# Performance work log

Hardware: AMD Instinct MI355X
Metric: run time of the kernel (lower is better)

The kernel has to match this reference:

```python
import jax, jax.numpy as jnp
import numpy as np

B, LQ, LK, D = 16, 2048, 2048, 64
TEMPERATURE = 8.0  # sqrt(d_k)


def setup_inputs() -> dict:
    key = jax.random.key(0)
    kq, kk, kv, km = jax.random.split(key, 4)
    q = jax.random.normal(kq, (B, LQ, D), dtype=jnp.float32)
    k = jax.random.normal(kk, (B, LK, D), dtype=jnp.float32)
    v = jax.random.normal(kv, (B, LK, D), dtype=jnp.float32)
    mask = jax.random.randint(km, (B, LQ, LK), 0, 2).astype(jnp.bool_)
    return {"q": q, "k": k, "v": v, "mask": mask}


def reference(q, k, v, mask):
    # attn = bmm(q, k^T) / temperature  -> [B, LQ, LK]
    attn = jnp.einsum("bqd,bkd->bqk", q, k) / TEMPERATURE
    attn = jnp.where(mask, -jnp.inf, attn)
    attn = jax.nn.softmax(attn, axis=2)
    out = jnp.einsum("bqk,bkd->bqd", attn, v)  # [B, LQ, D]
    return out, attn
```

## Files before the change

kernel.cpp:

```cpp
#include <hip/hip_runtime.h>
#include <hip/hip_bf16.h>

namespace {
constexpr int kB = 16;
constexpr int kLQ = 2048;
constexpr int kLK = 2048;
constexpr int kD = 64;
constexpr float kLog2e = 1.44269504088896340736f;
constexpr int kQT = 64;
constexpr int kKT = 512;
constexpr int kKStrB = 144;
constexpr int kMStrB = 40;
constexpr int kBStrB = 144;
constexpr int kChunk = 256;
constexpr int kEStrB = 528;
}

using short8 = __attribute__((ext_vector_type(8))) short;
using f32x4 = __attribute__((ext_vector_type(4))) float;

union S8U { short8 v; unsigned u[4]; };

static __device__ __forceinline__ unsigned pk2(float lo, float hi) {
    __hip_bfloat162 h = __float22bfloat162_rn(float2{lo, hi});
    unsigned short a = __builtin_bit_cast(unsigned short, h.x);
    unsigned short b = __builtin_bit_cast(unsigned short, h.y);
    return (unsigned)a | ((unsigned)b << 16);
}

__global__ __launch_bounds__(256, 4) void k1_qke(
    const float* __restrict__ qg, const float* __restrict__ kg,
    const void* __restrict__ maskg, float* __restrict__ attng,
    float* __restrict__ outg)
{
    __shared__ __align__(16) unsigned char s_kst[32 * kKStrB];
    __shared__ __align__(16) unsigned char s_mst[64 * kMStrB];
    __shared__ __align__(16) unsigned char s_bnc[4][16 * kBStrB];
    __shared__ int s_flag;

    const int tid = threadIdx.x;
    const int wave = tid >> 6;
    const int lane = tid & 63;
    const int r16 = lane & 15;
    const int g = lane >> 4;

    const int blk = blockIdx.x;
    const int b = blk >> 7;
    const int kt = (blk >> 5) & 3;
    const int qt = blk & 31;
    const int rows0 = qt * kQT;
    const int c0 = kt * kKT;

    if (tid < 64) {
        unsigned w = ((const unsigned*)maskg)[tid];
        unsigned long long bal = __ballot((w & 0xFFFFFF00u) != 0u);
        if (tid == 0) s_flag = (bal != 0ull) ? 1 : 0;
    }
    __syncthreads();
    const bool mask_byte = (s_flag != 0);
    const unsigned char* mask_u8 = (const unsigned char*)maskg;
    const int* mask_i32 = (const int*)maskg;

    short8 q0, q1;
    {
        const float4* qp = (const float4*)(qg + ((size_t)b * kLQ + rows0 + wave * 16 + r16) * kD);
        const float s = 0.125f * kLog2e;
        float4 x0 = qp[2*g + 0], x1 = qp[2*g + 1];
        float4 x2 = qp[2*g + 8], x3 = qp[2*g + 9];
        x0 *= s; x1 *= s; x2 *= s; x3 *= s;
        S8U a, c;
        a.u[0] = pk2(x0.x, x0.y); a.u[1] = pk2(x0.z, x0.w);
        a.u[2] = pk2(x1.x, x1.y); a.u[3] = pk2(x1.z, x1.w);
        c.u[0] = pk2(x2.x, x2.y); c.u[1] = pk2(x2.z, x2.w);
        c.u[2] = pk2(x3.x, x3.y); c.u[3] = pk2(x3.z, x3.w);
        q0 = a.v; q1 = c.v;
    }

    float wsum = 0.f;

    for (int sub = 0; sub < kKT / 32; ++sub) {
        const int csub = c0 + sub * 32;
        {
            const int krow = tid >> 3;
            const int d8 = (tid & 7) * 8;
            const float4* kp = (const float4*)(kg + ((size_t)b * kLK + csub + krow) * kD + d8);
            float4 y0 = kp[0], y1 = kp[1];
            S8U p;
            p.u[0] = pk2(y0.x, y0.y); p.u[1] = pk2(y0.z, y0.w);
            p.u[2] = pk2(y1.x, y1.y); p.u[3] = pk2(y1.z, y1.w);
            *(short8*)(s_kst + krow * kKStrB + d8 * 2) = p.v;
        }
        {
            const int mrow = tid >> 2;
            const int mc = (tid & 3) * 8;
            unsigned long long f;
            if (mask_byte) {
                f = *(const unsigned long long*)(mask_u8 +
                        ((size_t)b * kLQ + rows0 + mrow) * (size_t)kLK + csub + mc);
            } else {
                const int* mp = mask_i32 + ((size_t)b * kLQ + rows0 + mrow) * (size_t)kLK + csub + mc;
                const int4 m0 = *(const int4*)mp;
                const int4 m1 = *(const int4*)(mp + 4);
                f  = (m0.x ? 1ull : 0ull)       | (m0.y ? 1ull << 8 : 0ull)
                   | (m0.z ? 1ull << 16 : 0ull) | (m0.w ? 1ull << 24 : 0ull)
                   | (m1.x ? 1ull << 32 : 0ull) | (m1.y ? 1ull << 40 : 0ull)
                   | (m1.z ? 1ull << 48 : 0ull) | (m1.w ? 1ull << 56 : 0ull);
            }
            *(unsigned long long*)(s_mst + mrow * kMStrB + mc) = f;
        }
        __syncthreads();

        const short8 kA0 = *(const short8*)(s_kst + r16 * kKStrB + g * 16);
        const short8 kA1 = *(const short8*)(s_kst + r16 * kKStrB + 64 + g * 16);
        const short8 kB0 = *(const short8*)(s_kst + (16 + r16) * kKStrB + g * 16);
        const short8 kB1 = *(const short8*)(s_kst + (16 + r16) * kKStrB + 64 + g * 16);
        f32x4 accA = {0.f, 0.f, 0.f, 0.f}, accB = {0.f, 0.f, 0.f, 0.f};
        accA = __builtin_amdgcn_mfma_f32_16x16x32_bf16(kA0, q0, accA, 0, 0, 0);
        accA = __builtin_amdgcn_mfma_f32_16x16x32_bf16(kA1, q1, accA, 0, 0, 0);
        accB = __builtin_amdgcn_mfma_f32_16x16x32_bf16(kB0, q0, accB, 0, 0, 0);
        accB = __builtin_amdgcn_mfma_f32_16x16x32_bf16(kB1, q1, accB, 0, 0, 0);

        const unsigned mwA = *(const unsigned*)(s_mst + (wave * 16 + r16) * kMStrB + 4 * g);
        const unsigned mwB = *(const unsigned*)(s_mst + (wave * 16 + r16) * kMStrB + 16 + 4 * g);
        f32x4 eA, eB;
#pragma unroll
        for (int r = 0; r < 4; ++r) {
            eA[r] = ((mwA >> (8*r)) & 0xFFu) ? 0.f : __builtin_amdgcn_exp2f(accA[r]);
            eB[r] = ((mwB >> (8*r)) & 0xFFu) ? 0.f : __builtin_amdgcn_exp2f(accB[r]);
        }
        wsum += (eA[0] + eA[1]) + (eA[2] + eA[3]) + (eB[0] + eB[1]) + (eB[2] + eB[3]);
        *(f32x4*)(s_bnc[wave] + r16 * kBStrB + g * 16) = eA;
        *(f32x4*)(s_bnc[wave] + r16 * kBStrB + 64 + g * 16) = eB;
        __syncthreads();

        {
            const int row = tid >> 2;
            const int cseg = tid & 3;
            const unsigned char* src = s_bnc[row >> 4] + (row & 15) * kBStrB + cseg * 32;
            const f32x4 v0 = *(const f32x4*)src;
            const f32x4 v1 = *(const f32x4*)(src + 16);
            float* dst = attng + ((size_t)b * kLQ + rows0 + row) * (size_t)kLK + csub + cseg * 8;
            *(f32x4*)dst = v0;
            *(f32x4*)(dst + 4) = v1;
        }
    }
    wsum += __shfl_xor(wsum, 16, 64);
    wsum += __shfl_xor(wsum, 32, 64);
    if (g == 0)
        outg[((size_t)b * kLQ + rows0 + wave * 16 + r16) * kD + kt] = wsum;
}

__global__ __launch_bounds__(512, 2) void k2_norm_pv(
    const float* __restrict__ vg, float* __restrict__ attng,
    float* __restrict__ outg)
{
    __shared__ __align__(16) unsigned char s_e[16 * kEStrB];
    __shared__ float s_red[16][kD];
    __shared__ float s_rinv[16];

    const int tid = threadIdx.x;
    const int wave = tid >> 6;
    const int lane = tid & 63;
    const int r16 = lane & 15;
    const int g = lane >> 4;

    const int blk = blockIdx.x;
    const int b = blk >> 7;
    const int row0 = (blk & 127) * 16;

    if (tid < 64) {
        const int r = tid >> 2, p = tid & 3;
        float ps = outg[((size_t)b * kLQ + row0 + r) * kD + p];
        ps += __shfl_xor(ps, 1, 64);
        ps += __shfl_xor(ps, 2, 64);
        if (p == 0) s_rinv[r] = __builtin_amdgcn_rcpf(ps);
    }
    __syncthreads();

    const int d0 = (wave & 3) * 16;
    const int kh = wave >> 2;
    f32x4 acc = {0.f, 0.f, 0.f, 0.f};
    const float* vbase = vg + (size_t)b * kLK * kD + d0 + r16;

    for (int chunk = 0; chunk < kLK / kChunk; ++chunk) {
        const int c0 = chunk * kChunk;
        {
            const int row = tid >> 5;
            const int cc = tid & 31;
            const float rinv = s_rinv[row];
            float* ap = attng + ((size_t)b * kLQ + row0 + row) * (size_t)kLK + c0 + cc * 8;
            f32x4 e0 = *(const f32x4*)ap;
            f32x4 e1 = *(const f32x4*)(ap + 4);
            e0 *= rinv; e1 *= rinv;
            *(f32x4*)ap = e0;
            *(f32x4*)(ap + 4) = e1;
            S8U p;
            p.u[0] = pk2(e0[0], e0[1]); p.u[1] = pk2(e0[2], e0[3]);
            p.u[2] = pk2(e1[0], e1[1]); p.u[3] = pk2(e1[2], e1[3]);
            *(short8*)(s_e + row * kEStrB + cc * 16) = p.v;
        }
        __syncthreads();
#pragma unroll
        for (int s = 0; s < 4; ++s) {
            const int kk = kh * 128 + s * 32 + 8 * g;
            const short8 af = *(const short8*)(s_e + r16 * kEStrB + kk * 2);
            const float* vp = vbase + (size_t)(c0 + kk) * kD;
            float v0 = vp[0*kD], v1 = vp[1*kD], v2 = vp[2*kD], v3 = vp[3*kD];
            float v4 = vp[4*kD], v5 = vp[5*kD], v6 = vp[6*kD], v7 = vp[7*kD];
            S8U bv;
            bv.u[0] = pk2(v0, v1); bv.u[1] = pk2(v2, v3);
            bv.u[2] = pk2(v4, v5); bv.u[3] = pk2(v6, v7);
            acc = __builtin_amdgcn_mfma_f32_16x16x32_bf16(af, bv.v, acc, 0, 0, 0);
        }
        __syncthreads();
    }

    if (kh == 1) {
#pragma unroll
        for (int r = 0; r < 4; ++r) s_red[4*g + r][d0 + r16] = acc[r];
    }
    __syncthreads();
    if (kh == 0) {
#pragma unroll
        for (int r = 0; r < 4; ++r) {
            const int m = 4*g + r;
            outg[((size_t)b * kLQ + row0 + m) * kD + d0 + r16] = acc[r] + s_red[m][d0 + r16];
        }
    }
}

extern "C" void kernel_launch(void* const* d_in, const int* in_sizes, int n_in,
                              void* d_out, int out_size, void* d_ws, size_t ws_size,
                              hipStream_t stream) {
    (void)in_sizes; (void)n_in; (void)out_size; (void)d_ws; (void)ws_size;
    const float* q = (const float*)d_in[0];
    const float* k = (const float*)d_in[1];
    const float* v = (const float*)d_in[2];
    const void* mask = d_in[3];
    float* out = (float*)d_out;
    float* attn = out + (size_t)kB * kLQ * kD;
    k1_qke<<<dim3(kB * 128), 256, 0, stream>>>(q, k, mask, attn, out);
    k2_norm_pv<<<dim3(kB * 128), 512, 0, stream>>>(v, attn, out);
}
```

Before: 285.4 us.

## Stage unnormalized exp scores as bf16 in workspace instead of fp32 attn

The first kernel now packs the masked exp scores to bf16 and writes them to a workspace buffer, instead of writing fp32 into the attn output. The second kernel reads these half-size values, writes the normalized fp32 attn once, and feeds the raw bf16 values to the P·V MFMA. The output is rescaled by the row reciprocal at the end. This drops the fp32 read-modify-write round trip on the large attn matrix, cutting global traffic. In exchange the attn output now carries bf16 rounding, and the raised launch-bounds occupancy targets may force register spills.

```diff
diff --git a/kernel.cpp b/kernel.cpp
--- a/kernel.cpp
+++ b/kernel.cpp
@@ -11,7 +11,7 @@
 constexpr int kKT = 512;
 constexpr int kKStrB = 144;
 constexpr int kMStrB = 40;
-constexpr int kBStrB = 144;
+constexpr int kBStrB = 72;
 constexpr int kChunk = 256;
 constexpr int kEStrB = 528;
 }
@@ -27,10 +27,14 @@
     unsigned short b = __builtin_bit_cast(unsigned short, h.y);
     return (unsigned)a | ((unsigned)b << 16);
 }
-
-__global__ __launch_bounds__(256, 4) void k1_qke(
+static __device__ __forceinline__ float bf2f(unsigned short s) {
+    unsigned u = ((unsigned)s) << 16;
+    return __builtin_bit_cast(float, u);
+}
+
+__global__ __launch_bounds__(256, 8) void k1_qke(
     const float* __restrict__ qg, const float* __restrict__ kg,
-    const void* __restrict__ maskg, float* __restrict__ attng,
+    const void* __restrict__ maskg, unsigned short* __restrict__ ews,
     float* __restrict__ outg)
 {
     __shared__ __align__(16) unsigned char s_kst[32 * kKStrB];
@@ -122,26 +126,25 @@
 
         const unsigned mwA = *(const unsigned*)(s_mst + (wave * 16 + r16) * kMStrB + 4 * g);
         const unsigned mwB = *(const unsigned*)(s_mst + (wave * 16 + r16) * kMStrB + 16 + 4 * g);
-        f32x4 eA, eB;
+        float eA[4], eB[4];
 #pragma unroll
         for (int r = 0; r < 4; ++r) {
             eA[r] = ((mwA >> (8*r)) & 0xFFu) ? 0.f : __builtin_amdgcn_exp2f(accA[r]);
             eB[r] = ((mwB >> (8*r)) & 0xFFu) ? 0.f : __builtin_amdgcn_exp2f(accB[r]);
         }
         wsum += (eA[0] + eA[1]) + (eA[2] + eA[3]) + (eB[0] + eB[1]) + (eB[2] + eB[3]);
-        *(f32x4*)(s_bnc[wave] + r16 * kBStrB + g * 16) = eA;
-        *(f32x4*)(s_bnc[wave] + r16 * kBStrB + 64 + g * 16) = eB;
+        uint2 pA{ pk2(eA[0], eA[1]), pk2(eA[2], eA[3]) };
+        uint2 pB{ pk2(eB[0], eB[1]), pk2(eB[2], eB[3]) };
+        *(uint2*)(s_bnc[wave] + r16 * kBStrB + 8 * g) = pA;
+        *(uint2*)(s_bnc[wave] + r16 * kBStrB + 32 + 8 * g) = pB;
         __syncthreads();
 
         {
             const int row = tid >> 2;
-            const int cseg = tid & 3;
-            const unsigned char* src = s_bnc[row >> 4] + (row & 15) * kBStrB + cseg * 32;
-            const f32x4 v0 = *(const f32x4*)src;
-            const f32x4 v1 = *(const f32x4*)(src + 16);
-            float* dst = attng + ((size_t)b * kLQ + rows0 + row) * (size_t)kLK + csub + cseg * 8;
-            *(f32x4*)dst = v0;
-            *(f32x4*)(dst + 4) = v1;
+            const int seg = tid & 3;
+            const S8U* src = (const S8U*)(s_bnc[row >> 4] + (row & 15) * kBStrB + seg * 16);
+            unsigned short* dst = ews + ((size_t)b * kLQ + rows0 + row) * (size_t)kLK + csub + seg * 8;
+            *(short8*)dst = src->v;
         }
     }
     wsum += __shfl_xor(wsum, 16, 64);
@@ -150,9 +153,9 @@
         outg[((size_t)b * kLQ + rows0 + wave * 16 + r16) * kD + kt] = wsum;
 }
 
-__global__ __launch_bounds__(512, 2) void k2_norm_pv(
-    const float* __restrict__ vg, float* __restrict__ attng,
-    float* __restrict__ outg)
+__global__ __launch_bounds__(512, 8) void k2_norm_pv(
+    const float* __restrict__ vg, const unsigned short* __restrict__ ews,
+    float* __restrict__ attng, float* __restrict__ outg)
 {
     __shared__ __align__(16) unsigned char s_e[16 * kEStrB];
     __shared__ float s_red[16][kD];
@@ -188,16 +191,21 @@
             const int row = tid >> 5;
             const int cc = tid & 31;
             const float rinv = s_rinv[row];
+            const unsigned short* ep = ews + ((size_t)b * kLQ + row0 + row) * (size_t)kLK + c0 + cc * 8;
+            const short8 ev = *(const short8*)ep;
+            *(short8*)(s_e + row * kEStrB + cc * 16) = ev;
             float* ap = attng + ((size_t)b * kLQ + row0 + row) * (size_t)kLK + c0 + cc * 8;
-            f32x4 e0 = *(const f32x4*)ap;
-            f32x4 e1 = *(const f32x4*)(ap + 4);
-            e0 *= rinv; e1 *= rinv;
-            *(f32x4*)ap = e0;
-            *(f32x4*)(ap + 4) = e1;
-            S8U p;
-            p.u[0] = pk2(e0[0], e0[1]); p.u[1] = pk2(e0[2], e0[3]);
-            p.u[2] = pk2(e1[0], e1[1]); p.u[3] = pk2(e1[2], e1[3]);
-            *(short8*)(s_e + row * kEStrB + cc * 16) = p.v;
+            f32x4 a0, a1;
+            a0[0] = bf2f((unsigned short)ev[0]) * rinv;
+            a0[1] = bf2f((unsigned short)ev[1]) * rinv;
+            a0[2] = bf2f((unsigned short)ev[2]) * rinv;
+            a0[3] = bf2f((unsigned short)ev[3]) * rinv;
+            a1[0] = bf2f((unsigned short)ev[4]) * rinv;
+            a1[1] = bf2f((unsigned short)ev[5]) * rinv;
+            a1[2] = bf2f((unsigned short)ev[6]) * rinv;
+            a1[3] = bf2f((unsigned short)ev[7]) * rinv;
+            *(f32x4*)ap = a0;
+            *(f32x4*)(ap + 4) = a1;
         }
         __syncthreads();
 #pragma unroll
@@ -224,7 +232,8 @@
 #pragma unroll
         for (int r = 0; r < 4; ++r) {
             const int m = 4*g + r;
-            outg[((size_t)b * kLQ + row0 + m) * kD + d0 + r16] = acc[r] + s_red[m][d0 + r16];
+            outg[((size_t)b * kLQ + row0 + m) * kD + d0 + r16] =
+                (acc[r] + s_red[m][d0 + r16]) * s_rinv[m];
         }
     }
 }
@@ -232,13 +241,14 @@
 extern "C" void kernel_launch(void* const* d_in, const int* in_sizes, int n_in,
                               void* d_out, int out_size, void* d_ws, size_t ws_size,
                               hipStream_t stream) {
-    (void)in_sizes; (void)n_in; (void)out_size; (void)d_ws; (void)ws_size;
+    (void)in_sizes; (void)n_in; (void)out_size; (void)ws_size;
     const float* q = (const float*)d_in[0];
     const float* k = (const float*)d_in[1];
     const float* v = (const float*)d_in[2];
     const void* mask = d_in[3];
     float* out = (float*)d_out;
     float* attn = out + (size_t)kB * kLQ * kD;
-    k1_qke<<<dim3(kB * 128), 256, 0, stream>>>(q, k, mask, attn, out);
-    k2_norm_pv<<<dim3(kB * 128), 512, 0, stream>>>(v, attn, out);
-}
+    unsigned short* ews = (unsigned short*)d_ws;
+    k1_qke<<<dim3(kB * 128), 256, 0, stream>>>(q, k, mask, ews, out);
+    k2_norm_pv<<<dim3(kB * 128), 512, 0, stream>>>(v, ews, attn, out);
+}
```

Result: no change. 284.2 us (-0.4%).
